# Performance work log

Hardware: AMD Instinct MI355X
Metric: run time of the kernel (lower is better)

Reference implementation:

```python
import jax, jax.numpy as jnp
import numpy as np

H, L, N1, N2, N3 = 256, 141, 9, 34, 98
B, S = 64, 512

def setup_inputs() -> dict:
    key = jax.random.key(0)
    cnt = [0]
    def nrm(shape, s=0.05):
        cnt[0] += 1
        return jax.random.normal(jax.random.fold_in(key, cnt[0]), shape, jnp.float32) * s
    d = {}
    d['inputs'] = jax.random.randint(jax.random.fold_in(key, 1000), (B, S), 0, 30522)
    d['text_hidden'] = nrm((B, S, 768), 1.0)
    d['label_encoding'] = nrm((L, H), 1.0)
    d['w12'] = (jax.random.uniform(jax.random.fold_in(key, 1001), (N1, N2)) < 0.3).astype(jnp.float32)
    d['w23'] = (jax.random.uniform(jax.random.fold_in(key, 1002), (N2, N3)) < 0.3).astype(jnp.float32)
    d['fre12'] = jax.random.uniform(jax.random.fold_in(key, 1003), (N1, N2), jnp.float32)
    d['fre23'] = jax.random.uniform(jax.random.fold_in(key, 1004), (N2, N3), jnp.float32)
    for name in ['wi1', 'wf1', 'wo1', 'wu1', 'wi2', 'wf2', 'wo2', 'wu2']:
        d[name + '_W'] = nrm((H, H)); d[name + '_b'] = nrm((H,))
    for name in ['ui1', 'uf1', 'uo1', 'uu1', 'ui2', 'uf2', 'uo2', 'uu2']:
        d[name + '_W'] = nrm((H, H))
    d['mix_W'] = nrm((3 * H, H)); d['mix_b'] = nrm((H,))
    d['tt_W'] = nrm((768, H)); d['tt_b'] = nrm((H,))
    d['A'] = nrm((L, L)); d['Wp'] = nrm((H, H))
    d['out_W'] = nrm((L * H, L)); d['out_b'] = nrm((L,))
    return d

def reference(inputs, text_hidden, label_encoding, w12, w23, fre12, fre23,
              wi1_W, wi1_b, wf1_W, wf1_b, wo1_W, wo1_b, wu1_W, wu1_b,
              wi2_W, wi2_b, wf2_W, wf2_b, wo2_W, wo2_b, wu2_W, wu2_b,
              ui1_W, uf1_W, uo1_W, uu1_W, ui2_W, uf2_W, uo2_W, uu2_W,
              mix_W, mix_b, tt_W, tt_b, A, Wp, out_W, out_b):
    sig, tanh = jax.nn.sigmoid, jnp.tanh
    v1 = label_encoding[:N1]          # [N1,H]
    v2 = label_encoding[N1:N1 + N2]   # [N2,H]
    v3 = label_encoding[N1 + N2:]     # [N3,H]
    w21, w32 = w12.T, w23.T
    # --- top-down tree-LSTM (suffix 1) ---
    i11 = sig(v1 @ wi1_W + wi1_b); o11 = sig(v1 @ wo1_W + wo1_b); u11 = tanh(v1 @ wu1_W + wu1_b)
    c11 = i11 * u11; h11 = o11 * tanh(c11)
    h21t = w21 @ h11
    i21 = sig(v2 @ wi1_W + wi1_b + h21t @ ui1_W)
    f21 = sig(v2 @ wf1_W + wf1_b + h21t @ uf1_W)
    o21 = sig(v2 @ wo1_W + wo1_b + h21t @ uo1_W)
    u21 = tanh(v2 @ wu1_W + wu1_b + h21t @ uu1_W)
    c21 = i21 * u21 + f21 * (w21 @ c11); h21 = o21 * tanh(c21)
    h31t = w32 @ h21
    i31 = sig(v3 @ wi1_W + wi1_b + h31t @ ui1_W)
    f31 = sig(v3 @ wf1_W + wf1_b + h31t @ uf1_W)
    o31 = sig(v3 @ wo1_W + wo1_b + h31t @ uo1_W)
    u31 = tanh(v3 @ wu1_W + wu1_b + h31t @ uu1_W)
    c31 = i31 * u31 + f31 * (w32 @ c21); h31 = o31 * tanh(c31)
    # --- bottom-up tree-LSTM (suffix 2) ---
    i32 = sig(v3 @ wi2_W + wi2_b); o32 = sig(v3 @ wo2_W + wo2_b); u32 = tanh(v3 @ wu2_W + wu2_b)
    c32 = i32 * u32; h32 = o32 * tanh(c32)
    h22t = fre23 @ h32
    i22 = sig(v2 @ wi2_W + wi2_b + h22t @ ui2_W)
    f22 = sig((w32 @ v2) @ wf2_W + wf2_b + h32 @ uf2_W)   # [N3,H]
    o22 = sig(v2 @ wo2_W + wo2_b + h22t @ uo2_W)
    u22 = tanh(v2 @ wu2_W + wu2_b + h22t @ uu2_W)
    c22 = i22 * u22 + w23 @ (f22 * c32); h22 = o22 * tanh(c22)
    h12t = fre12 @ h22
    i12 = sig(v1 @ wi2_W + wi2_b + h12t @ ui2_W)
    f12 = sig((w21 @ v1) @ wf2_W + wf2_b + h22 @ uf2_W)   # [N2,H]
    o12 = sig(v1 @ wo2_W + wo2_b + h12t @ uo2_W)
    u12 = tanh(v1 @ wu2_W + wu2_b + h12t @ uu2_W)
    c12 = i12 * u12 + w12 @ (f12 * c22); h12 = o12 * tanh(c12)
    h1 = jnp.concatenate([h11, h12], axis=1)
    h2 = jnp.concatenate([h21, h22], axis=1)
    h3 = jnp.concatenate([h31, h32], axis=1)
    le = jnp.concatenate([h1, h2, h3], axis=0)            # [L,2H]
    temp = jax.nn.relu(A @ label_encoding @ Wp)           # [L,H]
    le = jnp.concatenate([le, temp], axis=1) @ mix_W + mix_b  # [L,H]
    # --- masked cross-attention pooling over text ---
    text = tanh(text_hidden @ tt_W + tt_b)                # [B,S,H]
    att = jnp.einsum('lh,bsh->bls', le, text)             # [B,L,S]
    pad = jnp.where((inputs == 0) | (inputs == 101) | (inputs == 102), -jnp.inf, 0.0).astype(text.dtype)
    att = jax.nn.softmax(att + pad[:, None, :], axis=2)
    features = jnp.einsum('bls,bsh->blh', att, text).reshape(inputs.shape[0], -1)  # [B,L*H]
    return sig(features @ out_W + out_b)                  # [B,L]
```

## Files before the change

### kernel.cpp

```cpp
#include <hip/hip_runtime.h>
#include <math.h>

static constexpr int H = 256, L = 141, N1 = 9, N2 = 34, N3 = 98;
static constexpr int B = 64, S = 512;

typedef __attribute__((ext_vector_type(8))) _Float16 f16x8;
typedef __attribute__((ext_vector_type(4))) float f32x4;

__device__ inline unsigned short f2h(float x) {
    _Float16 h = (_Float16)x;
    return __builtin_bit_cast(unsigned short, h);
}
__device__ inline float sigf(float x) { return 1.f / (1.f + __expf(-x)); }

__device__ inline void gload_lds16(const void* g, void* l) {
    __builtin_amdgcn_global_load_lds(
        (const __attribute__((address_space(1))) void*)g,
        (__attribute__((address_space(3))) void*)l, 16, 0, 0);
}

__global__ __launch_bounds__(256) void conv_ttW(
    const float* __restrict__ W, unsigned short* __restrict__ Bt)
{
    __shared__ unsigned short Tl[32][257];
    const int t = blockIdx.x, tid = threadIdx.x;
    #pragma unroll
    for (int p = 0; p < 32; p++) {
        int lin = p * 256 + tid;
        int r = lin >> 8, c = lin & 255;
        Tl[r][c] = f2h(W[(long)(t * 32 + r) * 256 + c]);
    }
    __syncthreads();
    unsigned short v[32];
    #pragma unroll
    for (int kin = 0; kin < 32; kin++) v[kin] = Tl[kin][tid];
    uint4* dst = (uint4*)(Bt + ((long)t * 256 + tid) * 32);
    #pragma unroll
    for (int q = 0; q < 4; q++) dst[q] = ((const uint4*)v)[q];
}

__global__ __launch_bounds__(512, 4) void text_gemm3(
    const float* __restrict__ Af,
    const unsigned short* __restrict__ Bt,
    const float* __restrict__ bias,
    unsigned short* __restrict__ outH,
    unsigned short* __restrict__ outHT)
{
    __shared__ unsigned short smem[28672];
// ... 103 lines not shown
            const int mlb = wm + i * 16 + quad * 4;
            const int n   = wn + j * 16 + l16;
            unsigned short hv[4];
            #pragma unroll
            for (int r = 0; r < 4; r++) {
                float v = tanhf(acc[i][j][r] + bv[j]);
                hv[r] = f2h(v);
                outH[(long)(m0 + mlb + r) * 256 + n] = hv[r];
            }
            uint2 p;
            p.x = hv[0] | ((unsigned int)hv[1] << 16);
            p.y = hv[2] | ((unsigned int)hv[3] << 16);
            *(uint2*)&T[n * 72 + mlb] = p;
        }
    }
    __syncthreads();
    {
        const int bb2 = m0 >> 9, s0 = m0 & 511;
        const int n = tid >> 1, half = tid & 1;
        const uint4* src = (const uint4*)&T[n * 72 + half * 32];
        uint4* dst = (uint4*)&outHT[((long)bb2 * 256 + n) * 512 + s0 + half * 32];
        dst[0] = src[0]; dst[1] = src[1];
        dst[2] = src[2]; dst[3] = src[3];
    }
}

__global__ __launch_bounds__(512, 4) void att_logits(
    const unsigned short* __restrict__ le_h,
    const unsigned short* __restrict__ text_h,
    const int* __restrict__ tokens,
    float* __restrict__ att)
{
    __shared__ unsigned short A_s[64 * 256];
    __shared__ unsigned short Bs[3][256 * 32];
    const int tid  = threadIdx.x;
    const int wave = tid >> 6, lane = tid & 63;
    const int quad = lane >> 4, l16 = lane & 15;
    const int s0 = blockIdx.x * 256;
    const int m0 = blockIdx.y * 64;
    const int b  = blockIdx.z;
    const int wm = (wave >> 2) * 32;
    const int wn = (wave & 3) * 64;

    const int bsc = (lane & 3) ^ ((lane >> 3) & 3);
    const long bOff0 = (long)(b * 512 + s0 + wave * 32 + (lane >> 2)) * 256 + bsc * 8;
    const long bOff1 = bOff0 + 16 * 256;
// ... 279 lines not shown

__global__ __launch_bounds__(256) void transp_t64(
    const float* __restrict__ src, unsigned short* __restrict__ dst,
    int R, int C)
{
    __shared__ unsigned short T[64 * 65];
    const int tid = threadIdx.x;
    const int r0 = blockIdx.x * 64, c0 = blockIdx.y * 64;
    #pragma unroll
    for (int p = 0; p < 16; p++) {
        int lin = p * 256 + tid;
        int r = lin >> 6, c = lin & 63;
        int gc = c0 + c;
        float v = (gc < C) ? src[(long)(r0 + r) * C + gc] : 0.f;
        T[c * 65 + r] = f2h(v);
    }
    __syncthreads();
    #pragma unroll
    for (int p = 0; p < 16; p++) {
        int lin = p * 256 + tid;
        int c = lin >> 6, r = lin & 63;
        if (c0 + c < C)
            dst[(long)(c0 + c) * R + r0 + r] = T[c * 65 + r];
    }
}

__global__ __launch_bounds__(256) void gate_pre(
    const float* __restrict__ le,
    const float* W0, const float* W1, const float* W2, const float* W3,
    const float* W4, const float* W5, const float* W6,
    const float* b0, const float* b1, const float* b2, const float* b3,
    const float* b4, const float* b5, const float* b6,
    float* __restrict__ G)
{
    __shared__ float ls[256];
    __shared__ float red[256];
    const int j = blockIdx.x >> 2, x = blockIdx.x & 3, m = blockIdx.y;
    const int tid = threadIdx.x, nl = tid & 63, ks = tid >> 6, n = x * 64 + nl;
    ls[tid] = le[(long)m * 256 + tid];
    __syncthreads();
    const float *W, *bb;
    switch (j) {
        case 0: W = W0; bb = b0; break;  case 1: W = W1; bb = b1; break;
        case 2: W = W2; bb = b2; break;  case 3: W = W3; bb = b3; break;
        case 4: W = W4; bb = b4; break;  case 5: W = W5; bb = b5; break;
        default: W = W6; bb = b6;
    }
    float a0 = 0, a1 = 0, a2 = 0, a3 = 0;
    for (int k = ks; k + 12 < 256; k += 16) {
        long o = (long)k * 256 + n;
        a0 += ls[k] * W[o];        a1 += ls[k + 4] * W[o + 1024];
        a2 += ls[k + 8] * W[o + 2048]; a3 += ls[k + 12] * W[o + 3072];
    }
    red[tid] = a0 + a1 + a2 + a3;
    __syncthreads();
    if (ks == 0)
        G[((long)j * 141 + m) * 256 + n] =
            red[nl] + red[64 + nl] + red[128 + nl] + red[192 + nl] + bb[n];
}

__global__ __launch_bounds__(256) void pre2(
    const float* __restrict__ A, const float* __restrict__ le,
    const float* __restrict__ w23, const float* __restrict__ w12,
    const float* __restrict__ Wp, const float* __restrict__ wf2_W,
    float* __restrict__ tmpP, float* __restrict__ wv2f, float* __restrict__ wv1f)
{
    __shared__ float cs[141];
    __shared__ float t[256];
    __shared__ float red[256];
    const int x = blockIdx.x, y = blockIdx.y;
    const int tid = threadIdx.x, nl = tid & 63, ks = tid >> 6, n = x * 64 + nl;
    int job, m, K1;
    if (y < 141)      { job = 0; m = y;       K1 = 141; }
    else if (y < 239) { job = 1; m = y - 141; K1 = 34; }
    else              { job = 2; m = y - 239; K1 = 9; }
    if (tid < K1)
        cs[tid] = (job == 0) ? A[(long)m * 141 + tid]
                : (job == 1) ? w23[(long)tid * 98 + m]
                             : w12[(long)tid * 34 + m];
    __syncthreads();
    const float* s1 = (job == 1) ? le + 9 * 256 : le;
    float acc = 0;
    #pragma unroll 4
    for (int k = 0; k < K1; k++) acc += cs[k] * s1[(long)k * 256 + tid];
    t[tid] = acc;
    __syncthreads();
    const float* W = (job == 0) ? Wp : wf2_W;
    float a0 = 0, a1 = 0, a2 = 0, a3 = 0;
    for (int k = ks; k + 12 < 256; k += 16) {
        long o = (long)k * 256 + n;
        a0 += t[k] * W[o];        a1 += t[k + 4] * W[o + 1024];
        a2 += t[k + 8] * W[o + 2048]; a3 += t[k + 12] * W[o + 3072];
    }
    red[tid] = a0 + a1 + a2 + a3;
    __syncthreads();
    if (ks == 0) {
        float tot = red[nl] + red[64 + nl] + red[128 + nl] + red[192 + nl];
        if (job == 0)      tmpP[(long)m * 256 + n] = fmaxf(tot, 0.f);
        else if (job == 1) wv2f[(long)m * 256 + n] = tot;
        else               wv1f[(long)m * 256 + n] = tot;
    }
}

__global__ __launch_bounds__(256) void ew1(
    const float* __restrict__ G, float* __restrict__ h11, float* __restrict__ c11,
    float* __restrict__ h32, float* __restrict__ c32)
{
    int y = blockIdx.x, n = threadIdx.x;
    if (y < 9) {
        int m = y;
        float iv = sigf(G[(0L * 141 + m) * 256 + n]);
        float ov = sigf(G[(2L * 141 + m) * 256 + n]);
        float uv = tanhf(G[(3L * 141 + m) * 256 + n]);
        float cv = iv * uv;
        c11[m * 256 + n] = cv; h11[m * 256 + n] = ov * tanhf(cv);
    } else {
        int r = y - 9, grow = 43 + r;
        float iv = sigf(G[(4L * 141 + grow) * 256 + n]);
        float ov = sigf(G[(5L * 141 + grow) * 256 + n]);
        float uv = tanhf(G[(6L * 141 + grow) * 256 + n]);
        float cv = iv * uv;
        c32[r * 256 + n] = cv; h32[r * 256 + n] = ov * tanhf(cv);
    }
}

__global__ __launch_bounds__(256) void chain_mm(int phase,
    const float* __restrict__ w12, const float* __restrict__ w23,
    const float* __restrict__ fre23, const float* __restrict__ fre12,
    const float* __restrict__ h11, const float* __restrict__ c11,
    const float* __restrict__ h32,
    const float* __restrict__ h21, const float* __restrict__ c21,
    const float* __restrict__ h22,
    const float* __restrict__ wv2f, const float* __restrict__ wv1f,
    const float* __restrict__ wf2_b, const float* __restrict__ uf2_W,
    const float* __restrict__ c32, const float* __restrict__ c22,
    float* __restrict__ h21t, float* __restrict__ c21p,
    float* __restrict__ h22t, float* __restrict__ fcb,
    float* __restrict__ h31t, float* __restrict__ c31p,
    float* __restrict__ h12t, float* __restrict__ fc2b)
{
    __shared__ float cs[256];
    __shared__ float red[256];
    const int x = blockIdx.x, y = blockIdx.y;
    const int tid = threadIdx.x, nl = tid & 63, ks = tid >> 6, n = x * 64 + nl;
    int job, m;
    if (phase == 0) {
        if (y < 34)       { job = 0; m = y; }
        else if (y < 68)  { job = 1; m = y - 34; }
        else if (y < 102) { job = 2; m = y - 68; }
        else              { job = 3; m = y - 102; }
    } else {
        if (y < 98)       { job = 0; m = y; }
        else if (y < 196) { job = 1; m = y - 98; }
        else if (y < 205) { job = 2; m = y - 196; }
        else              { job = 3; m = y - 205; }
    }
    if (job < 3) {
        int K; const float* src; float* dst;
        if (phase == 0) {
            K = (job == 2) ? 98 : 9;
            src = (job == 0) ? h11 : (job == 1) ? c11 : h32;
            dst = (job == 0) ? h21t : (job == 1) ? c21p : h22t;
            if (tid < K)
                cs[tid] = (job == 2) ? fre23[(long)m * 98 + tid]
                                     : w12[(long)tid * 34 + m];
        } else {
            K = 34;
            src = (job == 0) ? h21 : (job == 1) ? c21 : h22;
            dst = (job == 0) ? h31t : (job == 1) ? c31p : h12t;
            if (tid < K)
                cs[tid] = (job == 2) ? fre12[(long)m * 34 + tid]
                                     : w23[(long)tid * 98 + m];
        }
        __syncthreads();
        float a0 = 0;
        for (int k = ks; k < K; k += 4) a0 += cs[k] * src[(long)k * 256 + n];
        red[tid] = a0;
        __syncthreads();
        if (ks == 0)
            dst[(long)m * 256 + n] = red[nl] + red[64 + nl] + red[128 + nl] + red[192 + nl];
    } else {
        const float* row = (phase == 0) ? h32 + m * 256 : h22 + m * 256;
        const float* pre = (phase == 0) ? wv2f : wv1f;
        const float* cm  = (phase == 0) ? c32 : c22;
        float* dst       = (phase == 0) ? fcb : fc2b;
        cs[tid] = row[tid];
        __syncthreads();
        float a0 = 0, a1 = 0, a2 = 0, a3 = 0;
        for (int k = ks; k + 12 < 256; k += 16) {
            long o = (long)k * 256 + n;
            a0 += cs[k] * uf2_W[o];        a1 += cs[k + 4] * uf2_W[o + 1024];
            a2 += cs[k + 8] * uf2_W[o + 2048]; a3 += cs[k + 12] * uf2_W[o + 3072];
        }
        red[tid] = a0 + a1 + a2 + a3;
        __syncthreads();
        if (ks == 0) {
            float tot = red[nl] + red[64 + nl] + red[128 + nl] + red[192 + nl]
                      + pre[(long)m * 256 + n] + wf2_b[n];
            dst[(long)m * 256 + n] = sigf(tot) * cm[(long)m * 256 + n];
        }
    }
}

__global__ __launch_bounds__(256) void lstm_fused(int phase,
    const float* __restrict__ G,
    const float* __restrict__ h21t, const float* __restrict__ c21p,
    const float* __restrict__ h22t, const float* __restrict__ fcb,
    const float* __restrict__ h31t, const float* __restrict__ c31p,
    const float* __restrict__ h12t, const float* __restrict__ fc2b,
    const float* __restrict__ w23, const float* __restrict__ w12,
    const float* __restrict__ ui1, const float* __restrict__ uf1,
    const float* __restrict__ uo1, const float* __restrict__ uu1,
    const float* __restrict__ ui2, const float* __restrict__ uo2,
    const float* __restrict__ uu2,
    float* __restrict__ h21, float* __restrict__ c21,
    float* __restrict__ h22, float* __restrict__ c22,
    float* __restrict__ h31, float* __restrict__ h12)
{
    __shared__ float hs[256];
    __shared__ float cs[128];
    __shared__ float red[1024];
    const int x = blockIdx.x, y = blockIdx.y;
    const int tid = threadIdx.x, nl = tid & 63, ks = tid >> 6, n = x * 64 + nl;
    bool modef; int m, grow, Kx = 0;
    const float *hrow, *U0, *U1, *U2, *U3 = nullptr, *Sx = nullptr, *cmod = nullptr;
    float *ho, *co = nullptr;
    if (phase == 0) {
        if (y < 34) { modef = true;  m = y;      grow = 9 + m;  hrow = h21t;
                      U0 = ui1; U1 = uf1; U2 = uo1; U3 = uu1; cmod = c21p; ho = h21; co = c21; }
        else        { modef = false; m = y - 34; grow = 9 + m;  hrow = h22t;
                      U0 = ui2; U1 = uo2; U2 = uu2; Sx = fcb; Kx = 98; ho = h22; co = c22;
                      if (tid < 98) cs[tid] = w23[(long)m * 98 + tid]; }
    } else {
        if (y < 98) { modef = true;  m = y;      grow = 43 + m; hrow = h31t;
                      U0 = ui1; U1 = uf1; U2 = uo1; U3 = uu1; cmod = c31p; ho = h31; co = nullptr; }
        else        { modef = false; m = y - 98; grow = m;      hrow = h12t;
                      U0 = ui2; U1 = uo2; U2 = uu2; Sx = fc2b; Kx = 34; ho = h12; co = nullptr;
                      if (tid < 34) cs[tid] = w12[(long)m * 34 + tid]; }
    }
    hs[tid] = hrow[(long)m * 256 + tid];
    __syncthreads();
    float a0 = 0, a1 = 0, a2 = 0, a3 = 0;
    if (modef) {
        for (int k = ks; k < 256; k += 4) {
            float xv = hs[k]; long o = (long)k * 256 + n;
            a0 += xv * U0[o]; a1 += xv * U1[o]; a2 += xv * U2[o]; a3 += xv * U3[o];
        }
    } else {
        for (int k = ks; k < 256; k += 4) {
            float xv = hs[k]; long o = (long)k * 256 + n;
            a0 += xv * U0[o]; a1 += xv * U1[o]; a2 += xv * U2[o];
        }
        for (int k = ks; k < Kx; k += 4) a3 += cs[k] * Sx[(long)k * 256 + n];
    }
    red[tid] = a0; red[256 + tid] = a1; red[512 + tid] = a2; red[768 + tid] = a3;
    __syncthreads();
    if (ks == 0) {
        float t0 = 0, t1 = 0, t2 = 0, t3 = 0;
        #pragma unroll
        for (int s2 = 0; s2 < 4; s2++) {
            t0 += red[s2 * 64 + nl];       t1 += red[256 + s2 * 64 + nl];
            t2 += red[512 + s2 * 64 + nl]; t3 += red[768 + s2 * 64 + nl];
        }
        if (modef) {
            float ti = t0 + G[(0L * 141 + grow) * 256 + n];
            float tf = t1 + G[(1L * 141 + grow) * 256 + n];
            float to = t2 + G[(2L * 141 + grow) * 256 + n];
            float tu = t3 + G[(3L * 141 + grow) * 256 + n];
            float cv = sigf(ti) * tanhf(tu) + sigf(tf) * cmod[(long)m * 256 + n];
            ho[(long)m * 256 + n] = sigf(to) * tanhf(cv);
            if (co) co[(long)m * 256 + n] = cv;
        } else {
            float ti = t0 + G[(4L * 141 + grow) * 256 + n];
            float to = t1 + G[(5L * 141 + grow) * 256 + n];
            float tu = t2 + G[(6L * 141 + grow) * 256 + n];
            float cv = sigf(ti) * tanhf(tu) + t3;
            ho[(long)m * 256 + n] = sigf(to) * tanhf(cv);
            if (co) co[(long)m * 256 + n] = cv;
        }
    }
}

__global__ __launch_bounds__(256) void mix_mm(
    const float* __restrict__ h11, const float* __restrict__ h12,
    const float* __restrict__ h21, const float* __restrict__ h22,
    const float* __restrict__ h31, const float* __restrict__ h32,
    const float* __restrict__ tmpP, const float* __restrict__ mix_W,
    const float* __restrict__ mix_b, unsigned short* __restrict__ le_h)
{
    __shared__ float ls[768];
    __shared__ float red[256];
    const int x = blockIdx.x, l = blockIdx.y;
    const int tid = threadIdx.x, nl = tid & 63, ks = tid >> 6, n = x * 64 + nl;
    const float *pa, *pb; int r;
    if (l < 9)       { pa = h11; pb = h12; r = l; }
    else if (l < 43) { pa = h21; pb = h22; r = l - 9; }
    else             { pa = h31; pb = h32; r = l - 43; }
    for (int j = tid; j < 768; j += 256) {
        float v;
        if (j < 256)      v = pa[r * 256 + j];
        else if (j < 512) v = pb[r * 256 + (j - 256)];
        else              v = tmpP[l * 256 + (j - 512)];
        ls[j] = v;
    }
    __syncthreads();
    float a0 = 0, a1 = 0, a2 = 0, a3 = 0;
    for (int k = ks; k + 12 < 768; k += 16) {
        long o = (long)k * 256 + n;
        a0 += ls[k] * mix_W[o];        a1 += ls[k + 4] * mix_W[o + 1024];
        a2 += ls[k + 8] * mix_W[o + 2048]; a3 += ls[k + 12] * mix_W[o + 3072];
    }
    red[tid] = a0 + a1 + a2 + a3;
    __syncthreads();
    if (ks == 0) {
        float tot = red[nl] + red[64 + nl] + red[128 + nl] + red[192 + nl] + mix_b[n];
        le_h[(long)l * 256 + n] = f2h(tot);
    }
}

__global__ __launch_bounds__(256) void softmax512(
    const float* __restrict__ att, unsigned short* __restrict__ atth)
{
    __shared__ float red[256];
    const float* row = att + (long)blockIdx.x * 512;
    unsigned short* orow = atth + (long)blockIdx.x * 512;
    int t = threadIdx.x;
    float a = row[t], b = row[t + 256];
    red[t] = fmaxf(a, b);
    __syncthreads();
    for (int s = 128; s > 0; s >>= 1) {
        if (t < s) red[t] = fmaxf(red[t], red[t + s]);
        __syncthreads();
    }
    float m = red[0];
    __syncthreads();
    float ea = __expf(a - m), eb = __expf(b - m);
    red[t] = ea + eb;
    __syncthreads();
    for (int s = 128; s > 0; s >>= 1) {
// ... 51 lines not shown
    float* att     = ws; ws += (long)B * L * S;
    unsigned short* text_h  = (unsigned short*)ws; ws += (long)B * S * H / 2;
    unsigned short* text_hT = (unsigned short*)ws; ws += (long)B * S * H / 2;
    unsigned short* att_h   = (unsigned short*)ws; ws += (long)B * L * S / 2;
    unsigned short* tt_Wt   = (unsigned short*)ws; ws += 768 * H / 2;
    unsigned short* le_h    = (unsigned short*)ws; ws += L * H / 2 + 4;
    unsigned short* out_Wh  = (unsigned short*)ws; ws += (long)L * 36096 / 2;
    unsigned short* feat_h  = (unsigned short*)ws; ws += (long)B * L * H / 2;
    float* outacc = ws; ws += (long)B * L * 141;
    float* G    = ws; ws += 7 * 141 * 256;
    float* tmpP = ws; ws += L * H;
    float* wv2f = ws; ws += N3 * H;
    float* wv1f = ws; ws += N2 * H;
    float* h11  = ws; ws += N1 * H;  float* c11  = ws; ws += N1 * H;
    float* h21  = ws; ws += N2 * H;  float* c21  = ws; ws += N2 * H;
    float* h21t = ws; ws += N2 * H;  float* c21p = ws; ws += N2 * H;
    float* h31  = ws; ws += N3 * H;  float* h31t = ws; ws += N3 * H;
    float* c31p = ws; ws += N3 * H;
    float* h32  = ws; ws += N3 * H;  float* c32  = ws; ws += N3 * H;
    float* h22  = ws; ws += N2 * H;  float* c22  = ws; ws += N2 * H;
    float* h22t = ws; ws += N2 * H;  float* fcb  = ws; ws += N3 * H;
    float* h12  = ws; ws += N1 * H;  float* h12t = ws; ws += N1 * H;
    float* fc2b = ws; ws += N2 * H;

    conv_ttW<<<24, 256, 0, stream>>>(tt_W, tt_Wt);
    text_gemm3<<<512, 512, 0, stream>>>(
        text_hidden, tt_Wt, tt_b, text_h, text_hT);
    gate_pre<<<dim3(28, 141), 256, 0, stream>>>(label_enc,
        wi1_W, wf1_W, wo1_W, wu1_W, wi2_W, wo2_W, wu2_W,
        wi1_b, wf1_b, wo1_b, wu1_b, wi2_b, wo2_b, wu2_b, G);
    pre2<<<dim3(4, 273), 256, 0, stream>>>(Amat, label_enc, w23, w12, Wp, wf2_W,
        tmpP, wv2f, wv1f);
    transp_t64<<<dim3(36096 / 64, 3), 256, 0, stream>>>(out_W, out_Wh, 36096, 141);
    ew1<<<107, 256, 0, stream>>>(G, h11, c11, h32, c32);
    chain_mm<<<dim3(4, 200), 256, 0, stream>>>(0, w12, w23, fre23, fre12,
        h11, c11, h32, h21, c21, h22, wv2f, wv1f, wf2_b, uf2_W, c32, c22,
        h21t, c21p, h22t, fcb, h31t, c31p, h12t, fc2b);
    lstm_fused<<<dim3(4, 68), 256, 0, stream>>>(0, G,
        h21t, c21p, h22t, fcb, h31t, c31p, h12t, fc2b, w23, w12,
        ui1_W, uf1_W, uo1_W, uu1_W, ui2_W, uo2_W, uu2_W,
        h21, c21, h22, c22, h31, h12);
    chain_mm<<<dim3(4, 239), 256, 0, stream>>>(1, w12, w23, fre23, fre12,
        h11, c11, h32, h21, c21, h22, wv2f, wv1f, wf2_b, uf2_W, c32, c22,
        h21t, c21p, h22t, fcb, h31t, c31p, h12t, fc2b);
    lstm_fused<<<dim3(4, 107), 256, 0, stream>>>(1, G,
        h21t, c21p, h22t, fcb, h31t, c31p, h12t, fc2b, w23, w12,
        ui1_W, uf1_W, uo1_W, uu1_W, ui2_W, uo2_W, uu2_W,
        h21, c21, h22, c22, h31, h12);
    mix_mm<<<dim3(4, 141), 256, 0, stream>>>(h11, h12, h21, h22, h31, h32,
        tmpP, mix_W, mix_b, le_h);
    att_logits<<<dim3(2, 3, 64), 512, 0, stream>>>(
        le_h, text_h, inputs, att);
    softmax512<<<B * L, 256, 0, stream>>>(att, att_h);
    att_pv<<<dim3(3, 64), 512, 0, stream>>>(att_h, text_hT, feat_h);
    gemm_mfma<4, false, 2><<<dim3(2, 1, 141), 256, 0, stream>>>(
        feat_h, L * H, 0, out_Wh, L * H, 0, outacc, L, (long)B * L,
        B, L, L * H, nullptr, nullptr, nullptr, nullptr, 256);
    out_final<<<(B * L + 255) / 256, 256, 0, stream>>>(outacc, out_b, out, B * L, 141);
}
```

Measured before the change: 454.0 us.

## Fuse label-side tree-LSTM kernels into one persistent kernel with grid barriers

Replaces the eight small launches for the label tree-LSTM chain (gate_pre, pre2, ew1, two chain_mm, two lstm_fused, mix_mm) with a single persistent 512-block kernel. Stages are separated by atomic-counter grid barriers, and the counter is zeroed in conv_ttW. The goal is to remove launch overhead and the inter-kernel gaps on this latency-bound dependency chain. It relies on all 512 blocks being co-resident, otherwise the spin barrier deadlocks, and spinning blocks add overhead.

```diff
diff --git a/kernel.cpp b/kernel.cpp
--- a/kernel.cpp
+++ b/kernel.cpp
@@ -3,6 +3,7 @@
 
 static constexpr int H = 256, L = 141, N1 = 9, N2 = 34, N3 = 98;
 static constexpr int B = 64, S = 512;
+static constexpr int NB_LC = 512;
 
 typedef __attribute__((ext_vector_type(8))) _Float16 f16x8;
 typedef __attribute__((ext_vector_type(4))) float f32x4;
@@ -19,11 +20,25 @@
         (__attribute__((address_space(3))) void*)l, 16, 0, 0);
 }
 
+__device__ inline void gbar(int* cnt, int ph) {
+    __threadfence();
+    __syncthreads();
+    if (threadIdx.x == 0) {
+        atomicAdd(&cnt[ph], 1);
+        while (atomicAdd(&cnt[ph], 0) < NB_LC)
+            __builtin_amdgcn_s_sleep(1);
+    }
+    __syncthreads();
+    __threadfence();
+}
+
 __global__ __launch_bounds__(256) void conv_ttW(
-    const float* __restrict__ W, unsigned short* __restrict__ Bt)
+    const float* __restrict__ W, unsigned short* __restrict__ Bt,
+    int* __restrict__ cnt)
 {
     __shared__ unsigned short Tl[32][257];
     const int t = blockIdx.x, tid = threadIdx.x;
+    if (t == 0 && tid < 8) cnt[tid] = 0;
     #pragma unroll
     for (int p = 0; p < 32; p++) {
         int lin = p * 256 + tid;
@@ -173,6 +188,365 @@
         uint4* dst = (uint4*)&outHT[((long)bb2 * 256 + n) * 512 + s0 + half * 32];
         dst[0] = src[0]; dst[1] = src[1];
         dst[2] = src[2]; dst[3] = src[3];
+    }
+}
+
+__global__ __launch_bounds__(256) void label_chain(
+    const float* __restrict__ le,
+    const float* __restrict__ wi1_W, const float* __restrict__ wf1_W,
+    const float* __restrict__ wo1_W, const float* __restrict__ wu1_W,
+    const float* __restrict__ wi2_W, const float* __restrict__ wo2_W,
+    const float* __restrict__ wu2_W,
+    const float* __restrict__ wi1_b, const float* __restrict__ wf1_b,
+    const float* __restrict__ wo1_b, const float* __restrict__ wu1_b,
+    const float* __restrict__ wi2_b, const float* __restrict__ wo2_b,
+    const float* __restrict__ wu2_b,
+    const float* __restrict__ Amat, const float* __restrict__ w23,
+    const float* __restrict__ w12, const float* __restrict__ Wp,
+    const float* __restrict__ wf2_W, const float* __restrict__ wf2_b,
+    const float* __restrict__ fre23, const float* __restrict__ fre12,
+    const float* __restrict__ uf2_W,
+    const float* __restrict__ ui1, const float* __restrict__ uf1,
+    const float* __restrict__ uo1, const float* __restrict__ uu1,
+    const float* __restrict__ ui2, const float* __restrict__ uo2,
+    const float* __restrict__ uu2,
+    const float* __restrict__ mix_W, const float* __restrict__ mix_b,
+    float* __restrict__ G, float* __restrict__ tmpP,
+    float* __restrict__ wv2f, float* __restrict__ wv1f,
+    float* __restrict__ h11, float* __restrict__ c11,
+    float* __restrict__ h32, float* __restrict__ c32,
+    float* __restrict__ h21t, float* __restrict__ c21p,
+    float* __restrict__ h22t, float* __restrict__ fcb,
+    float* __restrict__ h21, float* __restrict__ c21,
+    float* __restrict__ h22, float* __restrict__ c22,
+    float* __restrict__ h31t, float* __restrict__ c31p,
+    float* __restrict__ h12t, float* __restrict__ fc2b,
+    float* __restrict__ h31, float* __restrict__ h12,
+    unsigned short* __restrict__ le_h,
+    int* __restrict__ cnt)
+{
+    __shared__ float smem[1408];
+    const int tid = threadIdx.x, bid = blockIdx.x;
+    const int nl = tid & 63, ks = tid >> 6;
+
+    for (int u = bid; u < 28 * 141; u += NB_LC) {
+        const int bx = u % 28, m = u / 28;
+        const int j = bx >> 2, x = bx & 3, n = x * 64 + nl;
+        float* ls = smem; float* red = smem + 256;
+        ls[tid] = le[(long)m * 256 + tid];
+        __syncthreads();
+        const float *W, *bb;
+        switch (j) {
+            case 0: W = wi1_W; bb = wi1_b; break;
+            case 1: W = wf1_W; bb = wf1_b; break;
+            case 2: W = wo1_W; bb = wo1_b; break;
+            case 3: W = wu1_W; bb = wu1_b; break;
+            case 4: W = wi2_W; bb = wi2_b; break;
+            case 5: W = wo2_W; bb = wo2_b; break;
+            default: W = wu2_W; bb = wu2_b;
+        }
+        float a0 = 0, a1 = 0, a2 = 0, a3 = 0;
+        for (int k = ks; k + 12 < 256; k += 16) {
+            long o = (long)k * 256 + n;
+            a0 += ls[k] * W[o];        a1 += ls[k + 4] * W[o + 1024];
+            a2 += ls[k + 8] * W[o + 2048]; a3 += ls[k + 12] * W[o + 3072];
+        }
+        red[tid] = a0 + a1 + a2 + a3;
+        __syncthreads();
+        if (ks == 0)
+            G[((long)j * 141 + m) * 256 + n] =
+                red[nl] + red[64 + nl] + red[128 + nl] + red[192 + nl] + bb[n];
+        __syncthreads();
+    }
+    for (int u = bid; u < 4 * 273; u += NB_LC) {
+        const int x = u % 4, y = u / 4, n = x * 64 + nl;
+        int job, m, K1;
+        if (y < 141)      { job = 0; m = y;       K1 = 141; }
+        else if (y < 239) { job = 1; m = y - 141; K1 = 34; }
+        else              { job = 2; m = y - 239; K1 = 9; }
+        float* cs = smem; float* t = smem + 256; float* red = smem + 512;
+        if (tid < K1)
+            cs[tid] = (job == 0) ? Amat[(long)m * 141 + tid]
+                    : (job == 1) ? w23[(long)tid * 98 + m]
+                                 : w12[(long)tid * 34 + m];
+        __syncthreads();
+        const float* s1 = (job == 1) ? le + 9 * 256 : le;
+        float acc = 0;
+        #pragma unroll 4
+        for (int k = 0; k < K1; k++) acc += cs[k] * s1[(long)k * 256 + tid];
+        t[tid] = acc;
+        __syncthreads();
+        const float* W = (job == 0) ? Wp : wf2_W;
+        float a0 = 0, a1 = 0, a2 = 0, a3 = 0;
+        for (int k = ks; k + 12 < 256; k += 16) {
+            long o = (long)k * 256 + n;
+            a0 += t[k] * W[o];        a1 += t[k + 4] * W[o + 1024];
+            a2 += t[k + 8] * W[o + 2048]; a3 += t[k + 12] * W[o + 3072];
+        }
+        red[tid] = a0 + a1 + a2 + a3;
+        __syncthreads();
+        if (ks == 0) {
+            float tot = red[nl] + red[64 + nl] + red[128 + nl] + red[192 + nl];
+            if (job == 0)      tmpP[(long)m * 256 + n] = fmaxf(tot, 0.f);
+            else if (job == 1) wv2f[(long)m * 256 + n] = tot;
+            else               wv1f[(long)m * 256 + n] = tot;
+        }
+        __syncthreads();
+    }
+    gbar(cnt, 0);
+
+    for (int y = bid; y < 107; y += NB_LC) {
+        const int n = tid;
+        if (y < 9) {
+            int m = y;
+            float iv = sigf(G[(0L * 141 + m) * 256 + n]);
+            float ov = sigf(G[(2L * 141 + m) * 256 + n]);
+            float uv = tanhf(G[(3L * 141 + m) * 256 + n]);
+            float cv = iv * uv;
+            c11[m * 256 + n] = cv; h11[m * 256 + n] = ov * tanhf(cv);
+        } else {
+            int r = y - 9, grow = 43 + r;
+            float iv = sigf(G[(4L * 141 + grow) * 256 + n]);
+            float ov = sigf(G[(5L * 141 + grow) * 256 + n]);
+            float uv = tanhf(G[(6L * 141 + grow) * 256 + n]);
+            float cv = iv * uv;
+            c32[r * 256 + n] = cv; h32[r * 256 + n] = ov * tanhf(cv);
+        }
+    }
+    gbar(cnt, 1);
+
+    for (int u = bid; u < 4 * 200; u += NB_LC) {
+        const int x = u % 4, y = u / 4, n = x * 64 + nl;
+        int job, m;
+        if (y < 34)       { job = 0; m = y; }
+        else if (y < 68)  { job = 1; m = y - 34; }
+        else if (y < 102) { job = 2; m = y - 68; }
+        else              { job = 3; m = y - 102; }
+        float* cs = smem; float* red = smem + 256;
+        if (job < 3) {
+            int K = (job == 2) ? 98 : 9;
+            const float* src = (job == 0) ? h11 : (job == 1) ? c11 : h32;
+            float* dst = (job == 0) ? h21t : (job == 1) ? c21p : h22t;
+            if (tid < K)
+                cs[tid] = (job == 2) ? fre23[(long)m * 98 + tid]
+                                     : w12[(long)tid * 34 + m];
+            __syncthreads();
+            float a0 = 0;
+            for (int k = ks; k < K; k += 4) a0 += cs[k] * src[(long)k * 256 + n];
+            red[tid] = a0;
+            __syncthreads();
+            if (ks == 0)
+                dst[(long)m * 256 + n] =
+                    red[nl] + red[64 + nl] + red[128 + nl] + red[192 + nl];
+            __syncthreads();
+        } else {
+            const float* row = h32 + m * 256;
+            cs[tid] = row[tid];
+            __syncthreads();
+            float a0 = 0, a1 = 0, a2 = 0, a3 = 0;
+            for (int k = ks; k + 12 < 256; k += 16) {
+                long o = (long)k * 256 + n;
+                a0 += cs[k] * uf2_W[o];        a1 += cs[k + 4] * uf2_W[o + 1024];
+                a2 += cs[k + 8] * uf2_W[o + 2048]; a3 += cs[k + 12] * uf2_W[o + 3072];
+            }
+            red[tid] = a0 + a1 + a2 + a3;
+            __syncthreads();
+            if (ks == 0) {
+                float tot = red[nl] + red[64 + nl] + red[128 + nl] + red[192 + nl]
+                          + wv2f[(long)m * 256 + n] + wf2_b[n];
+                fcb[(long)m * 256 + n] = sigf(tot) * c32[(long)m * 256 + n];
+            }
+            __syncthreads();
+        }
+    }
+    gbar(cnt, 2);
+
+    for (int u = bid; u < 4 * 68; u += NB_LC) {
+        const int x = u % 4, y = u / 4, n = x * 64 + nl;
+        float* hs = smem; float* cs2 = smem + 256; float* red = smem + 384;
+        bool modef; int m, grow, Kx = 0;
+        const float *hrow, *U0, *U1, *U2, *U3 = nullptr, *Sx = nullptr, *cmod = nullptr;
+        float *ho, *co = nullptr;
+        if (y < 34) { modef = true;  m = y;      grow = 9 + m;  hrow = h21t;
+                      U0 = ui1; U1 = uf1; U2 = uo1; U3 = uu1; cmod = c21p; ho = h21; co = c21; }
+        else        { modef = false; m = y - 34; grow = 9 + m;  hrow = h22t;
+                      U0 = ui2; U1 = uo2; U2 = uu2; Sx = fcb; Kx = 98; ho = h22; co = c22;
+                      if (tid < 98) cs2[tid] = w23[(long)m * 98 + tid]; }
+        hs[tid] = hrow[(long)m * 256 + tid];
+        __syncthreads();
+        float a0 = 0, a1 = 0, a2 = 0, a3 = 0;
+        if (modef) {
+            for (int k = ks; k < 256; k += 4) {
+                float xv = hs[k]; long o = (long)k * 256 + n;
+                a0 += xv * U0[o]; a1 += xv * U1[o]; a2 += xv * U2[o]; a3 += xv * U3[o];
+            }
+        } else {
+            for (int k = ks; k < 256; k += 4) {
+                float xv = hs[k]; long o = (long)k * 256 + n;
+                a0 += xv * U0[o]; a1 += xv * U1[o]; a2 += xv * U2[o];
+            }
+            for (int k = ks; k < Kx; k += 4) a3 += cs2[k] * Sx[(long)k * 256 + n];
+        }
+        red[tid] = a0; red[256 + tid] = a1; red[512 + tid] = a2; red[768 + tid] = a3;
+        __syncthreads();
+        if (ks == 0) {
+            float t0 = 0, t1 = 0, t2 = 0, t3 = 0;
+            #pragma unroll
+            for (int s2 = 0; s2 < 4; s2++) {
+                t0 += red[s2 * 64 + nl];       t1 += red[256 + s2 * 64 + nl];
+                t2 += red[512 + s2 * 64 + nl]; t3 += red[768 + s2 * 64 + nl];
+            }
+            if (modef) {
+                float ti = t0 + G[(0L * 141 + grow) * 256 + n];
+                float tf = t1 + G[(1L * 141 + grow) * 256 + n];
+                float to = t2 + G[(2L * 141 + grow) * 256 + n];
+                float tu = t3 + G[(3L * 141 + grow) * 256 + n];
+                float cv = sigf(ti) * tanhf(tu) + sigf(tf) * cmod[(long)m * 256 + n];
+                ho[(long)m * 256 + n] = sigf(to) * tanhf(cv);
+                if (co) co[(long)m * 256 + n] = cv;
+            } else {
+                float ti = t0 + G[(4L * 141 + grow) * 256 + n];
+                float to = t1 + G[(5L * 141 + grow) * 256 + n];
+                float tu = t2 + G[(6L * 141 + grow) * 256 + n];
+                float cv = sigf(ti) * tanhf(tu) + t3;
+                ho[(long)m * 256 + n] = sigf(to) * tanhf(cv);
+                if (co) co[(long)m * 256 + n] = cv;
+            }
+        }
+        __syncthreads();
+    }
+    gbar(cnt, 3);
+
+    for (int u = bid; u < 4 * 239; u += NB_LC) {
+        const int x = u % 4, y = u / 4, n = x * 64 + nl;
+        int job, m;
+        if (y < 98)       { job = 0; m = y; }
+        else if (y < 196) { job = 1; m = y - 98; }
+        else if (y < 205) { job = 2; m = y - 196; }
+        else              { job = 3; m = y - 205; }
+        float* cs = smem; float* red = smem + 256;
+        if (job < 3) {
+            int K = 34;
+            const float* src = (job == 0) ? h21 : (job == 1) ? c21 : h22;
+            float* dst = (job == 0) ? h31t : (job == 1) ? c31p : h12t;
+            if (tid < K)
+                cs[tid] = (job == 2) ? fre12[(long)m * 34 + tid]
+                                     : w23[(long)tid * 98 + m];
+            __syncthreads();
+            float a0 = 0;
+            for (int k = ks; k < K; k += 4) a0 += cs[k] * src[(long)k * 256 + n];
+            red[tid] = a0;
+            __syncthreads();
+            if (ks == 0)
+                dst[(long)m * 256 + n] =
+                    red[nl] + red[64 + nl] + red[128 + nl] + red[192 + nl];
+            __syncthreads();
+        } else {
+            const float* row = h22 + m * 256;
+            cs[tid] = row[tid];
+            __syncthreads();
+            float a0 = 0, a1 = 0, a2 = 0, a3 = 0;
+            for (int k = ks; k + 12 < 256; k += 16) {
+                long o = (long)k * 256 + n;
+                a0 += cs[k] * uf2_W[o];        a1 += cs[k + 4] * uf2_W[o + 1024];
+                a2 += cs[k + 8] * uf2_W[o + 2048]; a3 += cs[k + 12] * uf2_W[o + 3072];
+            }
+            red[tid] = a0 + a1 + a2 + a3;
+            __syncthreads();
+            if (ks == 0) {
+                float tot = red[nl] + red[64 + nl] + red[128 + nl] + red[192 + nl]
+                          + wv1f[(long)m * 256 + n] + wf2_b[n];
+                fc2b[(long)m * 256 + n] = sigf(tot) * c22[(long)m * 256 + n];
+            }
+            __syncthreads();
+        }
+    }
+    gbar(cnt, 4);
+
+    for (int u = bid; u < 4 * 107; u += NB_LC) {
+        const int x = u % 4, y = u / 4, n = x * 64 + nl;
+        float* hs = smem; float* cs2 = smem + 256; float* red = smem + 384;
+        bool modef; int m, grow, Kx = 0;
+        const float *hrow, *U0, *U1, *U2, *U3 = nullptr, *Sx = nullptr, *cmod = nullptr;
+        float *ho, *co = nullptr;
+        if (y < 98) { modef = true;  m = y;      grow = 43 + m; hrow = h31t;
+                      U0 = ui1; U1 = uf1; U2 = uo1; U3 = uu1; cmod = c31p; ho = h31; co = nullptr; }
+        else        { modef = false; m = y - 98; grow = m;      hrow = h12t;
+                      U0 = ui2; U1 = uo2; U2 = uu2; Sx = fc2b; Kx = 34; ho = h12; co = nullptr;
+                      if (tid < 34) cs2[tid] = w12[(long)m * 34 + tid]; }
+        hs[tid] = hrow[(long)m * 256 + tid];
+        __syncthreads();
+        float a0 = 0, a1 = 0, a2 = 0, a3 = 0;
+        if (modef) {
+            for (int k = ks; k < 256; k += 4) {
+                float xv = hs[k]; long o = (long)k * 256 + n;
+                a0 += xv * U0[o]; a1 += xv * U1[o]; a2 += xv * U2[o]; a3 += xv * U3[o];
+            }
+        } else {
+            for (int k = ks; k < 256; k += 4) {
+                float xv = hs[k]; long o = (long)k * 256 + n;
+                a0 += xv * U0[o]; a1 += xv * U1[o]; a2 += xv * U2[o];
+            }
+            for (int k = ks; k < Kx; k += 4) a3 += cs2[k] * Sx[(long)k * 256 + n];
+        }
+        red[tid] = a0; red[256 + tid] = a1; red[512 + tid] = a2; red[768 + tid] = a3;
+        __syncthreads();
+        if (ks == 0) {
+            float t0 = 0, t1 = 0, t2 = 0, t3 = 0;
+            #pragma unroll
+            for (int s2 = 0; s2 < 4; s2++) {
+                t0 += red[s2 * 64 + nl];       t1 += red[256 + s2 * 64 + nl];
+                t2 += red[512 + s2 * 64 + nl]; t3 += red[768 + s2 * 64 + nl];
+            }
+            if (modef) {
+                float ti = t0 + G[(0L * 141 + grow) * 256 + n];
+                float tf = t1 + G[(1L * 141 + grow) * 256 + n];
+                float to = t2 + G[(2L * 141 + grow) * 256 + n];
+                float tu = t3 + G[(3L * 141 + grow) * 256 + n];
+                float cv = sigf(ti) * tanhf(tu) + sigf(tf) * cmod[(long)m * 256 + n];
+                ho[(long)m * 256 + n] = sigf(to) * tanhf(cv);
+                if (co) co[(long)m * 256 + n] = cv;
+            } else {
+                float ti = t0 + G[(4L * 141 + grow) * 256 + n];
+                float to = t1 + G[(5L * 141 + grow) * 256 + n];
+                float tu = t2 + G[(6L * 141 + grow) * 256 + n];
+                float cv = sigf(ti) * tanhf(tu) + t3;
+                ho[(long)m * 256 + n] = sigf(to) * tanhf(cv);
+                if (co) co[(long)m * 256 + n] = cv;
+            }
+        }
+        __syncthreads();
+    }
+    gbar(cnt, 5);
+
+    for (int u = bid; u < 4 * 141; u += NB_LC) {
+        const int x = u % 4, l = u / 4, n = x * 64 + nl;
+        float* ls = smem; float* red = smem + 768;
+        const float *pa, *pb; int r;
+        if (l < 9)       { pa = h11; pb = h12; r = l; }
+        else if (l < 43) { pa = h21; pb = h22; r = l - 9; }
+        else             { pa = h31; pb = h32; r = l - 43; }
+        for (int j = tid; j < 768; j += 256) {
+            float v;
+            if (j < 256)      v = pa[r * 256 + j];
+            else if (j < 512) v = pb[r * 256 + (j - 256)];
+            else              v = tmpP[l * 256 + (j - 512)];
+            ls[j] = v;
+        }
+        __syncthreads();
+        float a0 = 0, a1 = 0, a2 = 0, a3 = 0;
+        for (int k = ks; k + 12 < 768; k += 16) {
+            long o = (long)k * 256 + n;
+            a0 += ls[k] * mix_W[o];        a1 += ls[k + 4] * mix_W[o + 1024];
+            a2 += ls[k + 8] * mix_W[o + 2048]; a3 += ls[k + 12] * mix_W[o + 3072];
+        }
+        red[tid] = a0 + a1 + a2 + a3;
+        __syncthreads();
+        if (ks == 0) {
+            float tot = red[nl] + red[64 + nl] + red[128 + nl] + red[192 + nl] + mix_b[n];
+            le_h[(long)l * 256 + n] = f2h(tot);
+        }
+        __syncthreads();
     }
 }
 
@@ -498,299 +872,6 @@
         int c = lin >> 6, r = lin & 63;
         if (c0 + c < C)
             dst[(long)(c0 + c) * R + r0 + r] = T[c * 65 + r];
-    }
-}
-
-__global__ __launch_bounds__(256) void gate_pre(
-    const float* __restrict__ le,
-    const float* W0, const float* W1, const float* W2, const float* W3,
-    const float* W4, const float* W5, const float* W6,
-    const float* b0, const float* b1, const float* b2, const float* b3,
-    const float* b4, const float* b5, const float* b6,
-    float* __restrict__ G)
-{
-    __shared__ float ls[256];
-    __shared__ float red[256];
-    const int j = blockIdx.x >> 2, x = blockIdx.x & 3, m = blockIdx.y;
-    const int tid = threadIdx.x, nl = tid & 63, ks = tid >> 6, n = x * 64 + nl;
-    ls[tid] = le[(long)m * 256 + tid];
-    __syncthreads();
-    const float *W, *bb;
-    switch (j) {
-        case 0: W = W0; bb = b0; break;  case 1: W = W1; bb = b1; break;
-        case 2: W = W2; bb = b2; break;  case 3: W = W3; bb = b3; break;
-        case 4: W = W4; bb = b4; break;  case 5: W = W5; bb = b5; break;
-        default: W = W6; bb = b6;
-    }
-    float a0 = 0, a1 = 0, a2 = 0, a3 = 0;
-    for (int k = ks; k + 12 < 256; k += 16) {
-        long o = (long)k * 256 + n;
-        a0 += ls[k] * W[o];        a1 += ls[k + 4] * W[o + 1024];
-        a2 += ls[k + 8] * W[o + 2048]; a3 += ls[k + 12] * W[o + 3072];
-    }
-    red[tid] = a0 + a1 + a2 + a3;
-    __syncthreads();
-    if (ks == 0)
-        G[((long)j * 141 + m) * 256 + n] =
-            red[nl] + red[64 + nl] + red[128 + nl] + red[192 + nl] + bb[n];
-}
-
-__global__ __launch_bounds__(256) void pre2(
-    const float* __restrict__ A, const float* __restrict__ le,
-    const float* __restrict__ w23, const float* __restrict__ w12,
-    const float* __restrict__ Wp, const float* __restrict__ wf2_W,
-    float* __restrict__ tmpP, float* __restrict__ wv2f, float* __restrict__ wv1f)
-{
-    __shared__ float cs[141];
-    __shared__ float t[256];
-    __shared__ float red[256];
-    const int x = blockIdx.x, y = blockIdx.y;
-    const int tid = threadIdx.x, nl = tid & 63, ks = tid >> 6, n = x * 64 + nl;
-    int job, m, K1;
-    if (y < 141)      { job = 0; m = y;       K1 = 141; }
-    else if (y < 239) { job = 1; m = y - 141; K1 = 34; }
-    else              { job = 2; m = y - 239; K1 = 9; }
-    if (tid < K1)
-        cs[tid] = (job == 0) ? A[(long)m * 141 + tid]
-                : (job == 1) ? w23[(long)tid * 98 + m]
-                             : w12[(long)tid * 34 + m];
-    __syncthreads();
-    const float* s1 = (job == 1) ? le + 9 * 256 : le;
-    float acc = 0;
-    #pragma unroll 4
-    for (int k = 0; k < K1; k++) acc += cs[k] * s1[(long)k * 256 + tid];
-    t[tid] = acc;
-    __syncthreads();
-    const float* W = (job == 0) ? Wp : wf2_W;
-    float a0 = 0, a1 = 0, a2 = 0, a3 = 0;
-    for (int k = ks; k + 12 < 256; k += 16) {
-        long o = (long)k * 256 + n;
-        a0 += t[k] * W[o];        a1 += t[k + 4] * W[o + 1024];
-        a2 += t[k + 8] * W[o + 2048]; a3 += t[k + 12] * W[o + 3072];
-    }
-    red[tid] = a0 + a1 + a2 + a3;
-    __syncthreads();
-    if (ks == 0) {
-        float tot = red[nl] + red[64 + nl] + red[128 + nl] + red[192 + nl];
-        if (job == 0)      tmpP[(long)m * 256 + n] = fmaxf(tot, 0.f);
-        else if (job == 1) wv2f[(long)m * 256 + n] = tot;
-        else               wv1f[(long)m * 256 + n] = tot;
-    }
-}
-
-__global__ __launch_bounds__(256) void ew1(
-    const float* __restrict__ G, float* __restrict__ h11, float* __restrict__ c11,
-    float* __restrict__ h32, float* __restrict__ c32)
-{
-    int y = blockIdx.x, n = threadIdx.x;
-    if (y < 9) {
-        int m = y;
-        float iv = sigf(G[(0L * 141 + m) * 256 + n]);
-        float ov = sigf(G[(2L * 141 + m) * 256 + n]);
-        float uv = tanhf(G[(3L * 141 + m) * 256 + n]);
-        float cv = iv * uv;
-        c11[m * 256 + n] = cv; h11[m * 256 + n] = ov * tanhf(cv);
-    } else {
-        int r = y - 9, grow = 43 + r;
-        float iv = sigf(G[(4L * 141 + grow) * 256 + n]);
-        float ov = sigf(G[(5L * 141 + grow) * 256 + n]);
-        float uv = tanhf(G[(6L * 141 + grow) * 256 + n]);
-        float cv = iv * uv;
-        c32[r * 256 + n] = cv; h32[r * 256 + n] = ov * tanhf(cv);
-    }
-}
-
-__global__ __launch_bounds__(256) void chain_mm(int phase,
-    const float* __restrict__ w12, const float* __restrict__ w23,
-    const float* __restrict__ fre23, const float* __restrict__ fre12,
-    const float* __restrict__ h11, const float* __restrict__ c11,
-    const float* __restrict__ h32,
-    const float* __restrict__ h21, const float* __restrict__ c21,
-    const float* __restrict__ h22,
-    const float* __restrict__ wv2f, const float* __restrict__ wv1f,
-    const float* __restrict__ wf2_b, const float* __restrict__ uf2_W,
-    const float* __restrict__ c32, const float* __restrict__ c22,
-    float* __restrict__ h21t, float* __restrict__ c21p,
-    float* __restrict__ h22t, float* __restrict__ fcb,
-    float* __restrict__ h31t, float* __restrict__ c31p,
-    float* __restrict__ h12t, float* __restrict__ fc2b)
-{
-    __shared__ float cs[256];
-    __shared__ float red[256];
-    const int x = blockIdx.x, y = blockIdx.y;
-    const int tid = threadIdx.x, nl = tid & 63, ks = tid >> 6, n = x * 64 + nl;
-    int job, m;
-    if (phase == 0) {
-        if (y < 34)       { job = 0; m = y; }
-        else if (y < 68)  { job = 1; m = y - 34; }
-        else if (y < 102) { job = 2; m = y - 68; }
-        else              { job = 3; m = y - 102; }
-    } else {
-        if (y < 98)       { job = 0; m = y; }
-        else if (y < 196) { job = 1; m = y - 98; }
-        else if (y < 205) { job = 2; m = y - 196; }
-        else              { job = 3; m = y - 205; }
-    }
-    if (job < 3) {
-        int K; const float* src; float* dst;
-        if (phase == 0) {
-            K = (job == 2) ? 98 : 9;
-            src = (job == 0) ? h11 : (job == 1) ? c11 : h32;
-            dst = (job == 0) ? h21t : (job == 1) ? c21p : h22t;
-            if (tid < K)
-                cs[tid] = (job == 2) ? fre23[(long)m * 98 + tid]
-                                     : w12[(long)tid * 34 + m];
-        } else {
-            K = 34;
-            src = (job == 0) ? h21 : (job == 1) ? c21 : h22;
-            dst = (job == 0) ? h31t : (job == 1) ? c31p : h12t;
-            if (tid < K)
-                cs[tid] = (job == 2) ? fre12[(long)m * 34 + tid]
-                                     : w23[(long)tid * 98 + m];
-        }
-        __syncthreads();
-        float a0 = 0;
-        for (int k = ks; k < K; k += 4) a0 += cs[k] * src[(long)k * 256 + n];
-        red[tid] = a0;
-        __syncthreads();
-        if (ks == 0)
-            dst[(long)m * 256 + n] = red[nl] + red[64 + nl] + red[128 + nl] + red[192 + nl];
-    } else {
-        const float* row = (phase == 0) ? h32 + m * 256 : h22 + m * 256;
-        const float* pre = (phase == 0) ? wv2f : wv1f;
-        const float* cm  = (phase == 0) ? c32 : c22;
-        float* dst       = (phase == 0) ? fcb : fc2b;
-        cs[tid] = row[tid];
-        __syncthreads();
-        float a0 = 0, a1 = 0, a2 = 0, a3 = 0;
-        for (int k = ks; k + 12 < 256; k += 16) {
-            long o = (long)k * 256 + n;
-            a0 += cs[k] * uf2_W[o];        a1 += cs[k + 4] * uf2_W[o + 1024];
-            a2 += cs[k + 8] * uf2_W[o + 2048]; a3 += cs[k + 12] * uf2_W[o + 3072];
-        }
-        red[tid] = a0 + a1 + a2 + a3;
-        __syncthreads();
-        if (ks == 0) {
-            float tot = red[nl] + red[64 + nl] + red[128 + nl] + red[192 + nl]
-                      + pre[(long)m * 256 + n] + wf2_b[n];
-            dst[(long)m * 256 + n] = sigf(tot) * cm[(long)m * 256 + n];
-        }
-    }
-}
-
-__global__ __launch_bounds__(256) void lstm_fused(int phase,
-    const float* __restrict__ G,
-    const float* __restrict__ h21t, const float* __restrict__ c21p,
-    const float* __restrict__ h22t, const float* __restrict__ fcb,
-    const float* __restrict__ h31t, const float* __restrict__ c31p,
-    const float* __restrict__ h12t, const float* __restrict__ fc2b,
-    const float* __restrict__ w23, const float* __restrict__ w12,
-    const float* __restrict__ ui1, const float* __restrict__ uf1,
-    const float* __restrict__ uo1, const float* __restrict__ uu1,
-    const float* __restrict__ ui2, const float* __restrict__ uo2,
-    const float* __restrict__ uu2,
-    float* __restrict__ h21, float* __restrict__ c21,
-    float* __restrict__ h22, float* __restrict__ c22,
-    float* __restrict__ h31, float* __restrict__ h12)
-{
-    __shared__ float hs[256];
-    __shared__ float cs[128];
-    __shared__ float red[1024];
-    const int x = blockIdx.x, y = blockIdx.y;
-    const int tid = threadIdx.x, nl = tid & 63, ks = tid >> 6, n = x * 64 + nl;
-    bool modef; int m, grow, Kx = 0;
-    const float *hrow, *U0, *U1, *U2, *U3 = nullptr, *Sx = nullptr, *cmod = nullptr;
-    float *ho, *co = nullptr;
-    if (phase == 0) {
-        if (y < 34) { modef = true;  m = y;      grow = 9 + m;  hrow = h21t;
-                      U0 = ui1; U1 = uf1; U2 = uo1; U3 = uu1; cmod = c21p; ho = h21; co = c21; }
-        else        { modef = false; m = y - 34; grow = 9 + m;  hrow = h22t;
-                      U0 = ui2; U1 = uo2; U2 = uu2; Sx = fcb; Kx = 98; ho = h22; co = c22;
-                      if (tid < 98) cs[tid] = w23[(long)m * 98 + tid]; }
-    } else {
-        if (y < 98) { modef = true;  m = y;      grow = 43 + m; hrow = h31t;
-                      U0 = ui1; U1 = uf1; U2 = uo1; U3 = uu1; cmod = c31p; ho = h31; co = nullptr; }
-        else        { modef = false; m = y - 98; grow = m;      hrow = h12t;
-                      U0 = ui2; U1 = uo2; U2 = uu2; Sx = fc2b; Kx = 34; ho = h12; co = nullptr;
-                      if (tid < 34) cs[tid] = w12[(long)m * 34 + tid]; }
-    }
-    hs[tid] = hrow[(long)m * 256 + tid];
-    __syncthreads();
-    float a0 = 0, a1 = 0, a2 = 0, a3 = 0;
-    if (modef) {
-        for (int k = ks; k < 256; k += 4) {
-            float xv = hs[k]; long o = (long)k * 256 + n;
-            a0 += xv * U0[o]; a1 += xv * U1[o]; a2 += xv * U2[o]; a3 += xv * U3[o];
-        }
-    } else {
-        for (int k = ks; k < 256; k += 4) {
-            float xv = hs[k]; long o = (long)k * 256 + n;
-            a0 += xv * U0[o]; a1 += xv * U1[o]; a2 += xv * U2[o];
-        }
-        for (int k = ks; k < Kx; k += 4) a3 += cs[k] * Sx[(long)k * 256 + n];
-    }
-    red[tid] = a0; red[256 + tid] = a1; red[512 + tid] = a2; red[768 + tid] = a3;
-    __syncthreads();
-    if (ks == 0) {
-        float t0 = 0, t1 = 0, t2 = 0, t3 = 0;
-        #pragma unroll
-        for (int s2 = 0; s2 < 4; s2++) {
-            t0 += red[s2 * 64 + nl];       t1 += red[256 + s2 * 64 + nl];
-            t2 += red[512 + s2 * 64 + nl]; t3 += red[768 + s2 * 64 + nl];
-        }
-        if (modef) {
-            float ti = t0 + G[(0L * 141 + grow) * 256 + n];
-            float tf = t1 + G[(1L * 141 + grow) * 256 + n];
-            float to = t2 + G[(2L * 141 + grow) * 256 + n];
-            float tu = t3 + G[(3L * 141 + grow) * 256 + n];
-            float cv = sigf(ti) * tanhf(tu) + sigf(tf) * cmod[(long)m * 256 + n];
-            ho[(long)m * 256 + n] = sigf(to) * tanhf(cv);
-            if (co) co[(long)m * 256 + n] = cv;
-        } else {
-            float ti = t0 + G[(4L * 141 + grow) * 256 + n];
-            float to = t1 + G[(5L * 141 + grow) * 256 + n];
-            float tu = t2 + G[(6L * 141 + grow) * 256 + n];
-            float cv = sigf(ti) * tanhf(tu) + t3;
-            ho[(long)m * 256 + n] = sigf(to) * tanhf(cv);
-            if (co) co[(long)m * 256 + n] = cv;
-        }
-    }
-}
-
-__global__ __launch_bounds__(256) void mix_mm(
-    const float* __restrict__ h11, const float* __restrict__ h12,
-    const float* __restrict__ h21, const float* __restrict__ h22,
-    const float* __restrict__ h31, const float* __restrict__ h32,
-    const float* __restrict__ tmpP, const float* __restrict__ mix_W,
-    const float* __restrict__ mix_b, unsigned short* __restrict__ le_h)
-{
-    __shared__ float ls[768];
-    __shared__ float red[256];
-    const int x = blockIdx.x, l = blockIdx.y;
-    const int tid = threadIdx.x, nl = tid & 63, ks = tid >> 6, n = x * 64 + nl;
-    const float *pa, *pb; int r;
-    if (l < 9)       { pa = h11; pb = h12; r = l; }
-    else if (l < 43) { pa = h21; pb = h22; r = l - 9; }
-    else             { pa = h31; pb = h32; r = l - 43; }
-    for (int j = tid; j < 768; j += 256) {
-        float v;
-        if (j < 256)      v = pa[r * 256 + j];
-        else if (j < 512) v = pb[r * 256 + (j - 256)];
-        else              v = tmpP[l * 256 + (j - 512)];
-        ls[j] = v;
-    }
-    __syncthreads();
-    float a0 = 0, a1 = 0, a2 = 0, a3 = 0;
-    for (int k = ks; k + 12 < 768; k += 16) {
-        long o = (long)k * 256 + n;
-        a0 += ls[k] * mix_W[o];        a1 += ls[k + 4] * mix_W[o + 1024];
-        a2 += ls[k + 8] * mix_W[o + 2048]; a3 += ls[k + 12] * mix_W[o + 3072];
-    }
-    red[tid] = a0 + a1 + a2 + a3;
-    __syncthreads();
-    if (ks == 0) {
-        float tot = red[nl] + red[64 + nl] + red[128 + nl] + red[192 + nl] + mix_b[n];
-        le_h[(long)l * 256 + n] = f2h(tot);
     }
 }
 
@@ -888,33 +969,21 @@
     float* h22t = ws; ws += N2 * H;  float* fcb  = ws; ws += N3 * H;
     float* h12  = ws; ws += N1 * H;  float* h12t = ws; ws += N1 * H;
     float* fc2b = ws; ws += N2 * H;
-
-    conv_ttW<<<24, 256, 0, stream>>>(tt_W, tt_Wt);
+    int* barcnt = (int*)ws; ws += 8;
+
+    conv_ttW<<<24, 256, 0, stream>>>(tt_W, tt_Wt, barcnt);
     text_gemm3<<<512, 512, 0, stream>>>(
         text_hidden, tt_Wt, tt_b, text_h, text_hT);
-    gate_pre<<<dim3(28, 141), 256, 0, stream>>>(label_enc,
+    transp_t64<<<dim3(36096 / 64, 3), 256, 0, stream>>>(out_W, out_Wh, 36096, 141);
+    label_chain<<<NB_LC, 256, 0, stream>>>(label_enc,
         wi1_W, wf1_W, wo1_W, wu1_W, wi2_W, wo2_W, wu2_W,
-        wi1_b, wf1_b, wo1_b, wu1_b, wi2_b, wo2_b, wu2_b, G);
-    pre2<<<dim3(4, 273), 256, 0, stream>>>(Amat, label_enc, w23, w12, Wp, wf2_W,
-        tmpP, wv2f, wv1f);
-    transp_t64<<<dim3(36096 / 64, 3), 256, 0, stream>>>(out_W, out_Wh, 36096, 141);
-    ew1<<<107, 256, 0, stream>>>(G, h11, c11, h32, c32);
-    chain_mm<<<dim3(4, 200), 256, 0, stream>>>(0, w12, w23, fre23, fre12,
-        h11, c11, h32, h21, c21, h22, wv2f, wv1f, wf2_b, uf2_W, c32, c22,
-        h21t, c21p, h22t, fcb, h31t, c31p, h12t, fc2b);
-    lstm_fused<<<dim3(4, 68), 256, 0, stream>>>(0, G,
-        h21t, c21p, h22t, fcb, h31t, c31p, h12t, fc2b, w23, w12,
+        wi1_b, wf1_b, wo1_b, wu1_b, wi2_b, wo2_b, wu2_b,
+        Amat, w23, w12, Wp, wf2_W, wf2_b, fre23, fre12, uf2_W,
         ui1_W, uf1_W, uo1_W, uu1_W, ui2_W, uo2_W, uu2_W,
-        h21, c21, h22, c22, h31, h12);
-    chain_mm<<<dim3(4, 239), 256, 0, stream>>>(1, w12, w23, fre23, fre12,
-        h11, c11, h32, h21, c21, h22, wv2f, wv1f, wf2_b, uf2_W, c32, c22,
-        h21t, c21p, h22t, fcb, h31t, c31p, h12t, fc2b);
-    lstm_fused<<<dim3(4, 107), 256, 0, stream>>>(1, G,
-        h21t, c21p, h22t, fcb, h31t, c31p, h12t, fc2b, w23, w12,
-        ui1_W, uf1_W, uo1_W, uu1_W, ui2_W, uo2_W, uu2_W,
-        h21, c21, h22, c22, h31, h12);
-    mix_mm<<<dim3(4, 141), 256, 0, stream>>>(h11, h12, h21, h22, h31, h32,
-        tmpP, mix_W, mix_b, le_h);
+        mix_W, mix_b,
+        G, tmpP, wv2f, wv1f, h11, c11, h32, c32,
+        h21t, c21p, h22t, fcb, h21, c21, h22, c22,
+        h31t, c31p, h12t, fc2b, h31, h12, le_h, barcnt);
     att_logits<<<dim3(2, 3, 64), 512, 0, stream>>>(
         le_h, text_h, inputs, att);
     softmax512<<<B * L, 256, 0, stream>>>(att, att_h);
```

New measurement: 1.003 ms. 2.21x slower.
